# Performance work log

Measured on AMD Instinct MI355X. Metric: run time of the kernel, lower is better.

## Reference

```python
import jax, jax.numpy as jnp
import numpy as np

HID = 2048   # hidden_size
H   = 16     # num_attention_heads
KV  = 8      # num_key_value_heads
D   = 128    # head_dim
T   = 2048   # total packed tokens
SW  = 512    # sliding_window
EPS = 1e-6
NEG = -1e30


def _rms(x, w, eps=EPS):
    # RMSNorm in fp32, optional learnable scale (w=None -> NoScale variant)
    x32 = x.astype(jnp.float32)
    var = jnp.mean(x32 * x32, axis=-1, keepdims=True)
    y = x32 * jax.lax.rsqrt(var + eps)
    if w is not None:
        y = w * y
    return y.astype(x.dtype)


def _rope(t, cos, sin):
    # t: [B,T,h,D]; cos/sin: [B,T,D] -> broadcast over head dim (unsqueeze_dim=2)
    c = cos[:, :, None, :]
    s = sin[:, :, None, :]
    d = c.shape[-1]
    tr, tp = t[..., :d], t[..., d:]
    half = d // 2
    rot = jnp.concatenate([-tr[..., half:], tr[..., :half]], axis=-1)
    return jnp.concatenate([tr * c + rot * s, tp], axis=-1)


def setup_inputs() -> dict:
    key = jax.random.key(0)
    ks = jax.random.split(key, 8)
    hidden_states = jax.random.normal(ks[0], (1, T, HID), dtype=jnp.float32)
    # realistic RoPE tables
    inv_freq = 1.0 / (10000.0 ** (np.arange(0, D, 2, dtype=np.float32) / D))
    pos = np.arange(T, dtype=np.float32)
    freqs = np.outer(pos, inv_freq)                 # [T, D/2]
    emb = np.concatenate([freqs, freqs], axis=-1)   # [T, D]
    cos = jnp.asarray(np.cos(emb))[None]            # [1, T, D]
    sin = jnp.asarray(np.sin(emb))[None]
    q_w = jax.random.normal(ks[1], (H * D, HID), dtype=jnp.float32) * 0.02
    k_w = jax.random.normal(ks[2], (KV * D, HID), dtype=jnp.float32) * 0.02
    v_w = jax.random.normal(ks[3], (KV * D, HID), dtype=jnp.float32) * 0.02
    o_w = jax.random.normal(ks[4], (HID, H * D), dtype=jnp.float32) * 0.02
    q_norm_w = 1.0 + 0.02 * jax.random.normal(ks[5], (D,), dtype=jnp.float32)
    k_norm_w = 1.0 + 0.02 * jax.random.normal(ks[6], (D,), dtype=jnp.float32)
    cu_seqlens = jnp.array([0, T // 2, T], dtype=jnp.int32)  # two packed seqs
    return dict(hidden_states=hidden_states, cos=cos, sin=sin,
                q_w=q_w, k_w=k_w, v_w=v_w, o_w=o_w,
                q_norm_w=q_norm_w, k_norm_w=k_norm_w,
                cu_seqlens=cu_seqlens, max_seqlen=T // 2)


def reference(hidden_states, cos, sin, q_w, k_w, v_w, o_w,
              q_norm_w, k_norm_w, cu_seqlens, max_seqlen):
    B, Ttot, _ = hidden_states.shape
    # QKV projections (no bias) + per-head RMSNorm + RoPE
    q = (hidden_states @ q_w.T).reshape(B, Ttot, H, D)
    q = _rope(_rms(q, q_norm_w), cos, sin)
    k = (hidden_states @ k_w.T).reshape(B, Ttot, KV, D)
    k = _rope(_rms(k, k_norm_w), cos, sin)
    v = (hidden_states @ v_w.T).reshape(B, Ttot, KV, D)
    v = _rms(v, None)  # value norm, no scale

    q0, k0, v0 = q[0], k[0], v[0]           # [T, h, D]
    n_rep = H // KV
    k0 = jnp.repeat(k0, n_rep, axis=1)      # GQA: repeat_interleave over heads
    v0 = jnp.repeat(v0, n_rep, axis=1)

    # block-diagonal (per packed sequence) causal sliding-window mask
    idx = jnp.arange(Ttot)
    seg = jnp.searchsorted(cu_seqlens, idx, side='right')  # segment id per token
    i, j = idx[:, None], idx[None, :]
    mask = (seg[:, None] == seg[None, :]) & (j <= i) & (i - j <= SW - 1)

    # softmax_scale = 1.0 (as in the source)
    scores = jnp.einsum('thd,shd->hts', q0, k0)            # [H, T, T]
    scores = jnp.where(mask[None], scores, NEG)
    probs = jax.nn.softmax(scores, axis=-1)
    attn = jnp.einsum('hts,shd->thd', probs, v0)           # [T, H, D]

    out = attn.reshape(1, Ttot, H * D) @ o_w.T             # o_proj
    return out
```

## Files before the change

### kernel.cpp

```cpp
#include <hip/hip_runtime.h>
#include <hip/hip_bf16.h>
#include <stdint.h>

#define T_TOK 2048
#define NH 16
#define NKV 8
#define HD 128
#define SW 512

typedef _Float16 f16x8 __attribute__((ext_vector_type(8)));
typedef _Float16 f16x4 __attribute__((ext_vector_type(4)));
typedef float f32x4 __attribute__((ext_vector_type(4)));

#define AS1 __attribute__((address_space(1)))
#define AS3 __attribute__((address_space(3)))

__global__ __launch_bounds__(256)
void cast_all(const float* __restrict__ hs, const float* __restrict__ qw,
              const float* __restrict__ kw, const float* __restrict__ vw,
              const float* __restrict__ ow,
              _Float16* __restrict__ hs16, _Float16* __restrict__ qw16,
              _Float16* __restrict__ kw16, _Float16* __restrict__ vw16,
              _Float16* __restrict__ ow16)
{
    const int b = blockIdx.x;
    const float* src; _Float16* dst; int base;
    if (b < 2048)      { src = hs; dst = hs16; base = b; }
    else if (b < 4096) { src = qw; dst = qw16; base = b - 2048; }
    else if (b < 5120) { src = kw; dst = kw16; base = b - 4096; }
    else if (b < 6144) { src = vw; dst = vw16; base = b - 5120; }
    else               { src = ow; dst = ow16; base = b - 6144; }
    const int i = (base * 256 + threadIdx.x) * 8;
    float4 f0 = *(const float4*)(src + i);
    float4 f1 = *(const float4*)(src + i + 4);
    f16x8 o;
    o[0] = (_Float16)f0.x; o[1] = (_Float16)f0.y; o[2] = (_Float16)f0.z; o[3] = (_Float16)f0.w;
    o[4] = (_Float16)f1.x; o[5] = (_Float16)f1.y; o[6] = (_Float16)f1.z; o[7] = (_Float16)f1.w;
    *(f16x8*)(dst + i) = o;
}

template<int OUT_F32>
__global__ __launch_bounds__(256)
void gemm_dma(const _Float16* __restrict__ A,
              const _Float16* __restrict__ B0,
              const _Float16* __restrict__ B1,
              const _Float16* __restrict__ B2,
              int split1, int split2,
              void* __restrict__ Cv,
              int K, int ldc)
{
    __shared__ __align__(16) _Float16 As[128 * 32];
    __shared__ __align__(16) _Float16 Bs[128 * 32];

    const int tid  = threadIdx.x;
    const int wave = tid >> 6;
    const int lane = tid & 63;
    const int bm = blockIdx.y * 128;
    const int bn = blockIdx.x * 128;
    const int wm = (wave >> 1) * 64;
    const int wn = (wave & 1) * 64;
    const int qd = lane >> 4;
    const int md = lane & 15;
    const int srow = lane >> 2;
    const int scol = (lane & 3) * 8;

    const _Float16* Bm;
    int bnb;
    if (bn >= split2)      { Bm = B2; bnb = bn - split2; }
    else if (bn >= split1) { Bm = B1; bnb = bn - split1; }
    else                   { Bm = B0; bnb = bn; }

    f32x4 acc[4][4] = {};

    for (int k0 = 0; k0 < K; k0 += 32) {
        __syncthreads();
        #pragma unroll
        for (int c = 0; c < 2; ++c) {
            const int chunk = wave * 2 + c;
            const _Float16* ga = A  + (size_t)(bm  + chunk * 16 + srow) * K + k0 + scol;
            const _Float16* gb = Bm + (size_t)(bnb + chunk * 16 + srow) * K + k0 + scol;
            __builtin_amdgcn_global_load_lds((const AS1 void*)ga, (AS3 void*)(&As[chunk * 512]), 16, 0, 0);
            __builtin_amdgcn_global_load_lds((const AS1 void*)gb, (AS3 void*)(&Bs[chunk * 512]), 16, 0, 0);
        }
        __syncthreads();

        f16x8 af[4], bg[4];
        #pragma unroll
        for (int i = 0; i < 4; ++i) {
            af[i] = *(const f16x8*)(&As[(wm + i * 16 + md) * 32 + qd * 8]);
            bg[i] = *(const f16x8*)(&Bs[(wn + i * 16 + md) * 32 + qd * 8]);
        }
        #pragma unroll
        for (int i = 0; i < 4; ++i) {
            #pragma unroll
            for (int j = 0; j < 4; ++j) {
                acc[i][j] = __builtin_amdgcn_mfma_f32_16x16x32_f16(af[i], bg[j], acc[i][j], 0, 0, 0);
            }
        }
    }

    #pragma unroll
    for (int i = 0; i < 4; ++i) {
        #pragma unroll
        for (int j = 0; j < 4; ++j) {
            #pragma unroll
            for (int r = 0; r < 4; ++r) {
                const int row = bm + wm + i * 16 + qd * 4 + r;
                const int col = bn + wn + j * 16 + md;
                if (OUT_F32) ((float*)Cv)[(size_t)row * ldc + col] = acc[i][j][r];
                else ((_Float16*)Cv)[(size_t)row * ldc + col] = (_Float16)acc[i][j][r];
            }
        }
    }
}

template<int A_F16, int OUT_F32>
__global__ __launch_bounds__(256)
void gemm_bt(const void* __restrict__ Av,
             const float* __restrict__ B0,
             const float* __restrict__ B1,
             const float* __restrict__ B2,
             int split1, int split2,
             void* __restrict__ Cv,
             int K, int ldc)
{
    __shared__ __align__(16) _Float16 As[128 * 40];
    __shared__ __align__(16) _Float16 Bs[128 * 40];

    const int tid  = threadIdx.x;
    const int wave = tid >> 6;
    const int lane = tid & 63;
    const int bm = blockIdx.y * 128;
    const int bn = blockIdx.x * 128;
    const int wm = (wave >> 1) * 64;
    const int wn = (wave & 1) * 64;
    const int qd = lane >> 4;
    const int md = lane & 15;

    const float* Bm;
    int bnb;
    if (bn >= split2)      { Bm = B2; bnb = bn - split2; }
    else if (bn >= split1) { Bm = B1; bnb = bn - split1; }
    else                   { Bm = B0; bnb = bn; }

    f32x4 acc[4][4] = {};

    for (int k0 = 0; k0 < K; k0 += 32) {
        f16x8 ra[2], rb[2];
        #pragma unroll
        for (int c = 0; c < 2; ++c) {
            const int e   = c * 256 + tid;
            const int row = e >> 2;
            const int col = (e & 3) * 8;
            if (A_F16) {
                ra[c] = *(const f16x8*)((const _Float16*)Av + (size_t)(bm + row) * K + k0 + col);
            } else {
                const float* ap = (const float*)Av + (size_t)(bm + row) * K + k0 + col;
                float4 f0 = *(const float4*)ap;
                float4 f1 = *(const float4*)(ap + 4);
                ra[c][0] = (_Float16)f0.x; ra[c][1] = (_Float16)f0.y;
                ra[c][2] = (_Float16)f0.z; ra[c][3] = (_Float16)f0.w;
                ra[c][4] = (_Float16)f1.x; ra[c][5] = (_Float16)f1.y;
                ra[c][6] = (_Float16)f1.z; ra[c][7] = (_Float16)f1.w;
            }
            {
                const float* bp = Bm + (size_t)(bnb + row) * K + k0 + col;
                float4 f0 = *(const float4*)bp;
                float4 f1 = *(const float4*)(bp + 4);
                rb[c][0] = (_Float16)f0.x; rb[c][1] = (_Float16)f0.y;
                rb[c][2] = (_Float16)f0.z; rb[c][3] = (_Float16)f0.w;
                rb[c][4] = (_Float16)f1.x; rb[c][5] = (_Float16)f1.y;
                rb[c][6] = (_Float16)f1.z; rb[c][7] = (_Float16)f1.w;
            }
        }
        __syncthreads();
        #pragma unroll
        for (int c = 0; c < 2; ++c) {
            const int e   = c * 256 + tid;
            const int row = e >> 2;
            const int col = (e & 3) * 8;
            *(f16x8*)(&As[row * 40 + col]) = ra[c];
            *(f16x8*)(&Bs[row * 40 + col]) = rb[c];
        }
        __syncthreads();

        f16x8 af[4], bg[4];
        #pragma unroll
        for (int i = 0; i < 4; ++i) {
            af[i] = *(const f16x8*)(&As[(wm + i * 16 + md) * 40 + qd * 8]);
            bg[i] = *(const f16x8*)(&Bs[(wn + i * 16 + md) * 40 + qd * 8]);
        }
        #pragma unroll
        for (int i = 0; i < 4; ++i) {
            #pragma unroll
            for (int j = 0; j < 4; ++j) {
                acc[i][j] = __builtin_amdgcn_mfma_f32_16x16x32_f16(af[i], bg[j], acc[i][j], 0, 0, 0);
            }
        }
    }

    #pragma unroll
    for (int i = 0; i < 4; ++i) {
        #pragma unroll
        for (int j = 0; j < 4; ++j) {
            #pragma unroll
            for (int r = 0; r < 4; ++r) {
                const int row = bm + wm + i * 16 + qd * 4 + r;
                const int col = bn + wn + j * 16 + md;
                if (OUT_F32) ((float*)Cv)[(size_t)row * ldc + col] = acc[i][j][r];
                else ((_Float16*)Cv)[(size_t)row * ldc + col] = (_Float16)acc[i][j][r];
            }
        }
    }
}

__global__ __launch_bounds__(256)
void norm_rope(const _Float16* __restrict__ qkv,
               const float* __restrict__ cosp,
               const float* __restrict__ sinp,
               const float* __restrict__ qnw,
               const float* __restrict__ knw,
               _Float16* __restrict__ qo,
               _Float16* __restrict__ ko)
{
    const unsigned idx  = blockIdx.x * 4 + (threadIdx.x >> 6);
    const int lane = threadIdx.x & 63;
    const int t = idx / 24;
    const int r = idx - t * 24;

    const size_t base = (size_t)t * 4096 + r * 128;
    float x0 = (float)qkv[base + lane];
    float x1 = (float)qkv[base + lane + 64];

    float ss = x0 * x0 + x1 * x1;
    #pragma unroll
    for (int s = 32; s; s >>= 1) ss += __shfl_xor(ss, s, 64);
    const float inv = rsqrtf(ss * (1.0f / 128.0f) + 1e-6f);
    float y0 = x0 * inv, y1 = x1 * inv;

    if (r < 16) { y0 *= qnw[lane]; y1 *= qnw[lane + 64]; }
    else        { y0 *= knw[lane]; y1 *= knw[lane + 64]; }

    const float c0 = cosp[t * 128 + lane];
    const float s0 = sinp[t * 128 + lane];
    const float c1 = cosp[t * 128 + lane + 64];
    const float s1 = sinp[t * 128 + lane + 64];
    const float o0 = y0 * c0 - y1 * s0;
    const float o1 = y1 * c1 + y0 * s1;

    const _Float16 b0 = (_Float16)o0, b1 = (_Float16)o1;
    if (r < 16) { _Float16* p = qo + ((size_t)t * NH  + r)        * HD; p[lane] = b0; p[lane + 64] = b1; }
    else        { _Float16* p = ko + ((size_t)t * NKV + (r - 16)) * HD; p[lane] = b0; p[lane + 64] = b1; }
}

__global__ __launch_bounds__(256)
void norm_v(const _Float16* __restrict__ qkv,
            _Float16* __restrict__ vt)
{
    __shared__ _Float16 tile[128 * 72];

    const int t0  = blockIdx.x * 64;
    const int kvh = blockIdx.y;
    const int tid = threadIdx.x;
    const int tok = tid >> 2;
    const int part = tid & 3;

    const _Float16* vp = qkv + (size_t)(t0 + tok) * 4096 + 3072 + kvh * 128 + part * 32;
    f16x8 raw[4];
    float x[32];
    float ss = 0.f;
    #pragma unroll
    for (int b = 0; b < 4; ++b) {
        raw[b] = *(const f16x8*)(vp + b * 8);
        #pragma unroll
        for (int j = 0; j < 8; ++j) { x[b*8+j] = (float)raw[b][j]; ss += x[b*8+j] * x[b*8+j]; }
    }
    ss += __shfl_xor(ss, 1, 64);
    ss += __shfl_xor(ss, 2, 64);
    const float inv = rsqrtf(ss * (1.0f / 128.0f) + 1e-6f);
    #pragma unroll
    for (int j = 0; j < 32; ++j) tile[(part * 32 + j) * 72 + tok] = (_Float16)(x[j] * inv);
    __syncthreads();

    const int d = tid >> 1, half = tid & 1;
    _Float16* op = vt + ((size_t)kvh * HD + d) * T_TOK + t0 + half * 32;
    #pragma unroll
    for (int j = 0; j < 4; ++j)
        *(f16x8*)(op + j * 8) = *(const f16x8*)(&tile[d * 72 + half * 32 + j * 8]);
}

__global__ __launch_bounds__(256)
void attn_mfma(const _Float16* __restrict__ q,
               const _Float16* __restrict__ k,
               const _Float16* __restrict__ vt,
               const int* __restrict__ cu,
               _Float16* __restrict__ attn)
{
    __shared__ __align__(16) _Float16 Ks[64 * 136];
    __shared__ __align__(16) _Float16 Vs[128 * 72];
    __shared__ __align__(16) _Float16 Ps[64 * 72];

    const int h   = blockIdx.y;
    const int kvh = h >> 1;
    const int t0  = blockIdx.x * 64;
    const int tid = threadIdx.x;
    const int w   = tid >> 6;
    const int lane = tid & 63;
    const int qd  = lane >> 4;
    const int md  = lane & 15;

    int seg_lo = (t0 >= cu[1]) ? cu[1] : cu[0];

    f16x8 qf[4];
    {
        const _Float16* qp = q + ((size_t)(t0 + w * 16 + md) * NH + h) * HD;
        #pragma unroll
        for (int ks = 0; ks < 4; ++ks) qf[ks] = *(const f16x8*)(qp + ks * 32 + qd * 8);
    }

    f32x4 O[8] = {};
    float mR[4], lR[4];
    #pragma unroll
    for (int r = 0; r < 4; ++r) { mR[r] = -1e30f; lR[r] = 0.f; }

    int blk_lo = t0 - (SW - 1); if (blk_lo < seg_lo) blk_lo = seg_lo;
    const int c_lo = blk_lo & ~63;

    for (int cs = c_lo; cs <= t0 + 63; cs += 64) {
        __syncthreads();
        #pragma unroll
        for (int g = 0; g < 4; ++g) {
            const int e = g * 256 + tid;
            const int key = e >> 4, d0 = (e & 15) * 8;
            *(f16x8*)(&Ks[key * 136 + d0]) =
                *(const f16x8*)(k + ((size_t)(cs + key) * NKV + kvh) * HD + d0);
        }
        #pragma unroll
        for (int g = 0; g < 4; ++g) {
            const int e = g * 256 + tid;
            const int d = e >> 3, c0 = (e & 7) * 8;
            *(f16x8*)(&Vs[d * 72 + c0]) =
                *(const f16x8*)(vt + ((size_t)kvh * HD + d) * T_TOK + cs + c0);
        }
        __syncthreads();

        f32x4 S[4] = {};
        #pragma unroll
        for (int nt = 0; nt < 4; ++nt) {
            #pragma unroll
            for (int ks = 0; ks < 4; ++ks) {
                f16x8 kf = *(const f16x8*)(&Ks[(nt * 16 + md) * 136 + ks * 32 + qd * 8]);
                S[nt] = __builtin_amdgcn_mfma_f32_16x16x32_f16(qf[ks], kf, S[nt], 0, 0, 0);
            }
        }

        const int rowb = t0 + w * 16 + qd * 4;
        float alpha[4];
        #pragma unroll
        for (int r = 0; r < 4; ++r) {
            const int rt = rowb + r;
            float mx = -1e30f;
            #pragma unroll
            for (int nt = 0; nt < 4; ++nt) {
                const int col = cs + nt * 16 + md;
                const bool ok = (col <= rt) && (col + (SW - 1) >= rt);
                const float s = ok ? S[nt][r] : -1e30f;
                S[nt][r] = s;
                mx = fmaxf(mx, s);
            }
            mx = fmaxf(mx, __shfl_xor(mx, 1, 64));
            mx = fmaxf(mx, __shfl_xor(mx, 2, 64));
            mx = fmaxf(mx, __shfl_xor(mx, 4, 64));
            mx = fmaxf(mx, __shfl_xor(mx, 8, 64));
            const float mn = fmaxf(mR[r], mx);
            alpha[r] = __expf(mR[r] - mn);
            mR[r] = mn;
        }

        #pragma unroll
        for (int r = 0; r < 4; ++r) {
            float rs = 0.f;
            #pragma unroll
            for (int nt = 0; nt < 4; ++nt) {
                const float p = __expf(S[nt][r] - mR[r]);
                S[nt][r] = p;
                rs += p;
            }
            rs += __shfl_xor(rs, 1, 64);
            rs += __shfl_xor(rs, 2, 64);
            rs += __shfl_xor(rs, 4, 64);
            rs += __shfl_xor(rs, 8, 64);
            lR[r] = lR[r] * alpha[r] + rs;
        }
        #pragma unroll
        for (int nt = 0; nt < 4; ++nt) {
            f16x4 p4;
            #pragma unroll
            for (int r = 0; r < 4; ++r) p4[r] = (_Float16)S[nt][r];
            *(f16x4*)(&Ps[(nt * 16 + md) * 72 + w * 16 + qd * 4]) = p4;
        }

        #pragma unroll
        for (int nt = 0; nt < 8; ++nt)
            #pragma unroll
            for (int r = 0; r < 4; ++r) O[nt][r] *= alpha[r];

        #pragma unroll
        for (int ks2 = 0; ks2 < 2; ++ks2) {
            f16x8 pf;
            #pragma unroll
            for (int j = 0; j < 8; ++j)
                pf[j] = Ps[(ks2 * 32 + qd * 8 + j) * 72 + w * 16 + md];
            #pragma unroll
            for (int nt = 0; nt < 8; ++nt) {
                f16x8 vf = *(const f16x8*)(&Vs[(nt * 16 + md) * 72 + ks2 * 32 + qd * 8]);
                O[nt] = __builtin_amdgcn_mfma_f32_16x16x32_f16(pf, vf, O[nt], 0, 0, 0);
            }
        }
    }

    float inv[4];
    #pragma unroll
    for (int r = 0; r < 4; ++r) inv[r] = 1.0f / lR[r];
    __syncthreads();
    #pragma unroll
    for (int nt = 0; nt < 8; ++nt)
        #pragma unroll
        for (int r = 0; r < 4; ++r)
            Ks[(w * 16 + qd * 4 + r) * 136 + nt * 16 + md] = (_Float16)(O[nt][r] * inv[r]);
    __syncthreads();
    #pragma unroll
    for (int g = 0; g < 4; ++g) {
        const int e = g * 256 + tid;
        const int row = e >> 4, d0 = (e & 15) * 8;
        *(f16x8*)(attn + ((size_t)(t0 + row) * NH + h) * HD + d0) =
            *(const f16x8*)(&Ks[row * 136 + d0]);
    }
}

extern "C" void kernel_launch(void* const* d_in, const int* in_sizes, int n_in,
                              void* d_out, int out_size, void* d_ws, size_t ws_size,
                              hipStream_t stream)
{
    const float* hs   = (const float*)d_in[0];
    const float* cosp = (const float*)d_in[1];
    const float* sinp = (const float*)d_in[2];
    const float* qw   = (const float*)d_in[3];
    const float* kw   = (const float*)d_in[4];
    const float* vw   = (const float*)d_in[5];
    const float* ow   = (const float*)d_in[6];
    const float* qnw  = (const float*)d_in[7];
    const float* knw  = (const float*)d_in[8];
    const int*   cu   = (const int*)d_in[9];
    float*       out  = (float*)d_out;

    _Float16* qkv   = (_Float16*)d_ws;
    _Float16* qb    = qkv  + (size_t)T_TOK * 4096;
    _Float16* kb    = qb   + (size_t)T_TOK * 2048;
    _Float16* vtb   = kb   + (size_t)T_TOK * 1024;
    _Float16* attnb = qkv;

    _Float16* hs16  = vtb  + (size_t)T_TOK * 1024;
    _Float16* qw16  = hs16 + (size_t)T_TOK * 2048;
    _Float16* kw16  = qw16 + (size_t)2048 * 2048;
    _Float16* vw16  = kw16 + (size_t)1024 * 2048;
    _Float16* ow16  = vw16 + (size_t)1024 * 2048;
    const size_t need = ((size_t)T_TOK * 4096 + T_TOK * 2048 + T_TOK * 1024 + T_TOK * 1024
                       + T_TOK * 2048 + 2048 * 2048 + 1024 * 2048 + 1024 * 2048 + 2048 * 2048)
                       * sizeof(_Float16);
    const bool precast = ws_size >= need;

    const dim3 blk(256);

    if (precast) {
        cast_all<<<8192, blk, 0, stream>>>(hs, qw, kw, vw, ow, hs16, qw16, kw16, vw16, ow16);
        gemm_dma<0><<<dim3(32, 16), blk, 0, stream>>>(hs16, qw16, kw16, vw16, 2048, 3072,
                                                      qkv, 2048, 4096);
    } else {
        gemm_bt<0, 0><<<dim3(32, 16), blk, 0, stream>>>(hs, qw, kw, vw, 2048, 3072,
                                                        qkv, 2048, 4096);
    }
    norm_rope<<<dim3((T_TOK * 24) / 4), blk, 0, stream>>>(qkv, cosp, sinp, qnw, knw, qb, kb);
    norm_v<<<dim3(T_TOK / 64, NKV), blk, 0, stream>>>(qkv, vtb);
    attn_mfma<<<dim3(T_TOK / 64, NH), blk, 0, stream>>>(qb, kb, vtb, cu, attnb);
    if (precast) {
        gemm_dma<1><<<dim3(16, 16), blk, 0, stream>>>(attnb, ow16, ow16, ow16, 1 << 30, 1 << 30,
                                                      out, 2048, 2048);
    } else {
        gemm_bt<1, 1><<<dim3(16, 16), blk, 0, stream>>>(attnb, ow, ow, ow, 1 << 30, 1 << 30,
                                                        out, 2048, 2048);
    }
}
```

Baseline: 266.4 us.

## Double-buffer GEMM LDS tiles and merge QK/V norm kernels into one launch

The DMA-based GEMM now keeps two LDS buffers, so the next K-slice is fetched by global_load_lds while MFMAs run on the current one. This cuts the loop from two barriers per iteration to one and hides global latency. Separately, the QK norm+RoPE and V norm+transpose kernels become one launch that branches on block index, saving a launch and a kernel boundary. The double buffer doubles LDS per block, which may lower occupancy. The prefetch also relies on the single trailing barrier to order the asynchronous LDS writes.

```diff
diff --git a/kernel.cpp b/kernel.cpp
--- a/kernel.cpp
+++ b/kernel.cpp
@@ -49,8 +49,8 @@
               void* __restrict__ Cv,
               int K, int ldc)
 {
-    __shared__ __align__(16) _Float16 As[128 * 32];
-    __shared__ __align__(16) _Float16 Bs[128 * 32];
+    __shared__ __align__(16) _Float16 As[2][128 * 32];
+    __shared__ __align__(16) _Float16 Bs[2][128 * 32];
 
     const int tid  = threadIdx.x;
     const int wave = tid >> 6;
@@ -72,23 +72,39 @@
 
     f32x4 acc[4][4] = {};
 
-    for (int k0 = 0; k0 < K; k0 += 32) {
-        __syncthreads();
-        #pragma unroll
-        for (int c = 0; c < 2; ++c) {
-            const int chunk = wave * 2 + c;
-            const _Float16* ga = A  + (size_t)(bm  + chunk * 16 + srow) * K + k0 + scol;
-            const _Float16* gb = Bm + (size_t)(bnb + chunk * 16 + srow) * K + k0 + scol;
-            __builtin_amdgcn_global_load_lds((const AS1 void*)ga, (AS3 void*)(&As[chunk * 512]), 16, 0, 0);
-            __builtin_amdgcn_global_load_lds((const AS1 void*)gb, (AS3 void*)(&Bs[chunk * 512]), 16, 0, 0);
-        }
-        __syncthreads();
+    const _Float16* aBase = A  + (size_t)(bm  + wave * 32 + srow) * K + scol;
+    const _Float16* bBase = Bm + (size_t)(bnb + wave * 32 + srow) * K + scol;
+
+    const int nIter = K / 32;
+    #pragma unroll
+    for (int c = 0; c < 2; ++c) {
+        const int chunk = wave * 2 + c;
+        __builtin_amdgcn_global_load_lds((const AS1 void*)(aBase + (size_t)c * 16 * K),
+                                         (AS3 void*)(&As[0][chunk * 512]), 16, 0, 0);
+        __builtin_amdgcn_global_load_lds((const AS1 void*)(bBase + (size_t)c * 16 * K),
+                                         (AS3 void*)(&Bs[0][chunk * 512]), 16, 0, 0);
+    }
+    __syncthreads();
+
+    for (int it = 0; it < nIter; ++it) {
+        const int buf = it & 1;
+        if (it + 1 < nIter) {
+            const int k1 = (it + 1) * 32;
+            #pragma unroll
+            for (int c = 0; c < 2; ++c) {
+                const int chunk = wave * 2 + c;
+                __builtin_amdgcn_global_load_lds((const AS1 void*)(aBase + (size_t)c * 16 * K + k1),
+                                                 (AS3 void*)(&As[buf ^ 1][chunk * 512]), 16, 0, 0);
+                __builtin_amdgcn_global_load_lds((const AS1 void*)(bBase + (size_t)c * 16 * K + k1),
+                                                 (AS3 void*)(&Bs[buf ^ 1][chunk * 512]), 16, 0, 0);
+            }
+        }
 
         f16x8 af[4], bg[4];
         #pragma unroll
         for (int i = 0; i < 4; ++i) {
-            af[i] = *(const f16x8*)(&As[(wm + i * 16 + md) * 32 + qd * 8]);
-            bg[i] = *(const f16x8*)(&Bs[(wn + i * 16 + md) * 32 + qd * 8]);
+            af[i] = *(const f16x8*)(&As[buf][(wm + i * 16 + md) * 32 + qd * 8]);
+            bg[i] = *(const f16x8*)(&Bs[buf][(wn + i * 16 + md) * 32 + qd * 8]);
         }
         #pragma unroll
         for (int i = 0; i < 4; ++i) {
@@ -97,6 +113,7 @@
                 acc[i][j] = __builtin_amdgcn_mfma_f32_16x16x32_f16(af[i], bg[j], acc[i][j], 0, 0, 0);
             }
         }
+        __syncthreads();
     }
 
     #pragma unroll
@@ -214,79 +231,79 @@
     }
 }
 
+#define QKB ((T_TOK * 24) / 4)
 __global__ __launch_bounds__(256)
-void norm_rope(const _Float16* __restrict__ qkv,
-               const float* __restrict__ cosp,
-               const float* __restrict__ sinp,
-               const float* __restrict__ qnw,
-               const float* __restrict__ knw,
-               _Float16* __restrict__ qo,
-               _Float16* __restrict__ ko)
-{
-    const unsigned idx  = blockIdx.x * 4 + (threadIdx.x >> 6);
-    const int lane = threadIdx.x & 63;
-    const int t = idx / 24;
-    const int r = idx - t * 24;
-
-    const size_t base = (size_t)t * 4096 + r * 128;
-    float x0 = (float)qkv[base + lane];
-    float x1 = (float)qkv[base + lane + 64];
-
-    float ss = x0 * x0 + x1 * x1;
-    #pragma unroll
-    for (int s = 32; s; s >>= 1) ss += __shfl_xor(ss, s, 64);
-    const float inv = rsqrtf(ss * (1.0f / 128.0f) + 1e-6f);
-    float y0 = x0 * inv, y1 = x1 * inv;
-
-    if (r < 16) { y0 *= qnw[lane]; y1 *= qnw[lane + 64]; }
-    else        { y0 *= knw[lane]; y1 *= knw[lane + 64]; }
-
-    const float c0 = cosp[t * 128 + lane];
-    const float s0 = sinp[t * 128 + lane];
-    const float c1 = cosp[t * 128 + lane + 64];
-    const float s1 = sinp[t * 128 + lane + 64];
-    const float o0 = y0 * c0 - y1 * s0;
-    const float o1 = y1 * c1 + y0 * s1;
-
-    const _Float16 b0 = (_Float16)o0, b1 = (_Float16)o1;
-    if (r < 16) { _Float16* p = qo + ((size_t)t * NH  + r)        * HD; p[lane] = b0; p[lane + 64] = b1; }
-    else        { _Float16* p = ko + ((size_t)t * NKV + (r - 16)) * HD; p[lane] = b0; p[lane + 64] = b1; }
-}
-
-__global__ __launch_bounds__(256)
-void norm_v(const _Float16* __restrict__ qkv,
-            _Float16* __restrict__ vt)
+void norm_all(const _Float16* __restrict__ qkv,
+              const float* __restrict__ cosp,
+              const float* __restrict__ sinp,
+              const float* __restrict__ qnw,
+              const float* __restrict__ knw,
+              _Float16* __restrict__ qo,
+              _Float16* __restrict__ ko,
+              _Float16* __restrict__ vt)
 {
     __shared__ _Float16 tile[128 * 72];
-
-    const int t0  = blockIdx.x * 64;
-    const int kvh = blockIdx.y;
     const int tid = threadIdx.x;
-    const int tok = tid >> 2;
-    const int part = tid & 3;
-
-    const _Float16* vp = qkv + (size_t)(t0 + tok) * 4096 + 3072 + kvh * 128 + part * 32;
-    f16x8 raw[4];
-    float x[32];
-    float ss = 0.f;
-    #pragma unroll
-    for (int b = 0; b < 4; ++b) {
-        raw[b] = *(const f16x8*)(vp + b * 8);
-        #pragma unroll
-        for (int j = 0; j < 8; ++j) { x[b*8+j] = (float)raw[b][j]; ss += x[b*8+j] * x[b*8+j]; }
-    }
-    ss += __shfl_xor(ss, 1, 64);
-    ss += __shfl_xor(ss, 2, 64);
-    const float inv = rsqrtf(ss * (1.0f / 128.0f) + 1e-6f);
-    #pragma unroll
-    for (int j = 0; j < 32; ++j) tile[(part * 32 + j) * 72 + tok] = (_Float16)(x[j] * inv);
-    __syncthreads();
-
-    const int d = tid >> 1, half = tid & 1;
-    _Float16* op = vt + ((size_t)kvh * HD + d) * T_TOK + t0 + half * 32;
-    #pragma unroll
-    for (int j = 0; j < 4; ++j)
-        *(f16x8*)(op + j * 8) = *(const f16x8*)(&tile[d * 72 + half * 32 + j * 8]);
+
+    if (blockIdx.x < QKB) {
+        const unsigned idx  = blockIdx.x * 4 + (tid >> 6);
+        const int lane = tid & 63;
+        const int t = idx / 24;
+        const int r = idx - t * 24;
+
+        const size_t base = (size_t)t * 4096 + r * 128;
+        float x0 = (float)qkv[base + lane];
+        float x1 = (float)qkv[base + lane + 64];
+
+        float ss = x0 * x0 + x1 * x1;
+        #pragma unroll
+        for (int s = 32; s; s >>= 1) ss += __shfl_xor(ss, s, 64);
+        const float inv = rsqrtf(ss * (1.0f / 128.0f) + 1e-6f);
+        float y0 = x0 * inv, y1 = x1 * inv;
+
+        if (r < 16) { y0 *= qnw[lane]; y1 *= qnw[lane + 64]; }
+        else        { y0 *= knw[lane]; y1 *= knw[lane + 64]; }
+
+        const float c0 = cosp[t * 128 + lane];
+        const float s0 = sinp[t * 128 + lane];
+        const float c1 = cosp[t * 128 + lane + 64];
+        const float s1 = sinp[t * 128 + lane + 64];
+        const float o0 = y0 * c0 - y1 * s0;
+        const float o1 = y1 * c1 + y0 * s1;
+
+        const _Float16 b0 = (_Float16)o0, b1 = (_Float16)o1;
+        if (r < 16) { _Float16* p = qo + ((size_t)t * NH  + r)        * HD; p[lane] = b0; p[lane + 64] = b1; }
+        else        { _Float16* p = ko + ((size_t)t * NKV + (r - 16)) * HD; p[lane] = b0; p[lane + 64] = b1; }
+    } else {
+        const int bv  = blockIdx.x - QKB;
+        const int t0  = (bv & 31) * 64;
+        const int kvh = bv >> 5;
+        const int tok = tid >> 2;
+        const int part = tid & 3;
+
+        const _Float16* vp = qkv + (size_t)(t0 + tok) * 4096 + 3072 + kvh * 128 + part * 32;
+        f16x8 raw[4];
+        float x[32];
+        float ss = 0.f;
+        #pragma unroll
+        for (int b = 0; b < 4; ++b) {
+            raw[b] = *(const f16x8*)(vp + b * 8);
+            #pragma unroll
+            for (int j = 0; j < 8; ++j) { x[b*8+j] = (float)raw[b][j]; ss += x[b*8+j] * x[b*8+j]; }
+        }
+        ss += __shfl_xor(ss, 1, 64);
+        ss += __shfl_xor(ss, 2, 64);
+        const float inv = rsqrtf(ss * (1.0f / 128.0f) + 1e-6f);
+        #pragma unroll
+        for (int j = 0; j < 32; ++j) tile[(part * 32 + j) * 72 + tok] = (_Float16)(x[j] * inv);
+        __syncthreads();
+
+        const int d = tid >> 1, half = tid & 1;
+        _Float16* op = vt + ((size_t)kvh * HD + d) * T_TOK + t0 + half * 32;
+        #pragma unroll
+        for (int j = 0; j < 4; ++j)
+            *(f16x8*)(op + j * 8) = *(const f16x8*)(&tile[d * 72 + half * 32 + j * 8]);
+    }
 }
 
 __global__ __launch_bounds__(256)
@@ -480,8 +497,7 @@
         gemm_bt<0, 0><<<dim3(32, 16), blk, 0, stream>>>(hs, qw, kw, vw, 2048, 3072,
                                                         qkv, 2048, 4096);
     }
-    norm_rope<<<dim3((T_TOK * 24) / 4), blk, 0, stream>>>(qkv, cosp, sinp, qnw, knw, qb, kb);
-    norm_v<<<dim3(T_TOK / 64, NKV), blk, 0, stream>>>(qkv, vtb);
+    norm_all<<<dim3(QKB + 256), blk, 0, stream>>>(qkv, cosp, sinp, qnw, knw, qb, kb, vtb);
     attn_mfma<<<dim3(T_TOK / 64, NH), blk, 0, stream>>>(qb, kb, vtb, cu, attnb);
     if (precast) {
         gemm_dma<1><<<dim3(16, 16), blk, 0, stream>>>(attnb, ow16, ow16, ow16, 1 << 30, 1 << 30,
```

After: 254.1 us. 1.05x faster.
